# Kernel tuning notes

Measured on AMD Instinct MI355X. Metric: run time of the kernel, lower is better.

Reference implementation:

```python
import jax, jax.numpy as jnp
import numpy as np
import math

B, S, CTX, D, H, DH = 2, 2048, 256, 1024, 16, 64
INNER = H * DH
DFF = 4 * D


def layernorm(x, eps=1e-5):
    m = jnp.mean(x, axis=-1, keepdims=True)
    v = jnp.var(x, axis=-1, keepdims=True)
    return (x - m) * jax.lax.rsqrt(v + eps)


def adaln(x, t, w, b):
    # AdaLayerNorm: linear(t) -> (scale, shift); NOTE: original never applies SiLU.
    emb = t @ w + b                       # [B,1,2D]
    scale, shift = jnp.split(emb, 2, axis=-1)
    return layernorm(x) * (1.0 + scale) + shift


def mha(xq, ctx, wq, wk, wv, wo, bo):
    b, sq, _ = xq.shape
    sk = ctx.shape[1]
    q = (xq @ wq).reshape(b, sq, H, DH).transpose(0, 2, 1, 3)   # bhqd
    k = (ctx @ wk).reshape(b, sk, H, DH).transpose(0, 2, 1, 3)  # bhkd
    v = (ctx @ wv).reshape(b, sk, H, DH).transpose(0, 2, 1, 3)
    scores = jnp.einsum('bhqd,bhkd->bhqk', q, k) / math.sqrt(DH)
    attn = jax.nn.softmax(scores, axis=-1)
    out = jnp.einsum('bhqk,bhkd->bhqd', attn, v)
    out = out.transpose(0, 2, 1, 3).reshape(b, sq, INNER)
    return out @ wo + bo


def glu_ff(x, w1, b1, w2, b2):
    u = x @ w1 + b1                       # [B,S,2*DFF]
    a, gate = jnp.split(u, 2, axis=-1)
    return (a * jax.nn.gelu(gate, approximate=False)) @ w2 + b2


def setup_inputs():
    key = jax.random.key(0)
    ks = jax.random.split(key, 24)
    s = 1.0 / math.sqrt(D)

    def n(k, shape, scale=1.0):
        return jax.random.normal(k, shape, dtype=jnp.float32) * scale

    return {
        'x': n(ks[0], (B, S, D)),
        't': n(ks[1], (B, 1, D)),
        'context': n(ks[2], (B, CTX, D)),
        # self-attention (attn1)
        'attn1_wq': n(ks[3], (D, INNER), s),
        'attn1_wk': n(ks[4], (D, INNER), s),
        'attn1_wv': n(ks[5], (D, INNER), s),
        'attn1_wo': n(ks[6], (INNER, D), s),
        'attn1_bo': n(ks[7], (D,), 0.01),
        # cross-attention (attn2)
        'attn2_wq': n(ks[8], (D, INNER), s),
        'attn2_wk': n(ks[9], (D, INNER), s),
        'attn2_wv': n(ks[10], (D, INNER), s),
        'attn2_wo': n(ks[11], (INNER, D), s),
        'attn2_bo': n(ks[12], (D,), 0.01),
        # gated FFN
        'ff_w1': n(ks[13], (D, 2 * DFF), s),
        'ff_b1': n(ks[14], (2 * DFF,), 0.01),
        'ff_w2': n(ks[15], (DFF, D), 1.0 / math.sqrt(DFF)),
        'ff_b2': n(ks[16], (D,), 0.01),
        # AdaLayerNorm linears (D -> 2D)
        'norm1_w': n(ks[17], (D, 2 * D), s),
        'norm1_b': n(ks[18], (2 * D,), 0.01),
        'norm2_w': n(ks[19], (D, 2 * D), s),
        'norm2_b': n(ks[20], (2 * D,), 0.01),
        'norm3_w': n(ks[21], (D, 2 * D), s),
        'norm3_b': n(ks[22], (2 * D,), 0.01),
    }


def reference(x, t, context,
              attn1_wq, attn1_wk, attn1_wv, attn1_wo, attn1_bo,
              attn2_wq, attn2_wk, attn2_wv, attn2_wo, attn2_bo,
              ff_w1, ff_b1, ff_w2, ff_b2,
              norm1_w, norm1_b, norm2_w, norm2_b, norm3_w, norm3_b):
    h1 = adaln(x, t, norm1_w, norm1_b)
    x = mha(h1, h1, attn1_wq, attn1_wk, attn1_wv, attn1_wo, attn1_bo) + x
    h2 = adaln(x, t, norm2_w, norm2_b)
    x = mha(h2, context, attn2_wq, attn2_wk, attn2_wv, attn2_wo, attn2_bo) + x
    h3 = adaln(x, t, norm3_w, norm3_b)
    x = glu_ff(h3, ff_w1, ff_b1, ff_w2, ff_b2) + x
    return x
```

## Files before the change

### kernel.cpp

```cpp
#include <hip/hip_runtime.h>
#include <hip/hip_bf16.h>
#include <math.h>
#include <stdint.h>

typedef __bf16 bf16;
typedef __attribute__((ext_vector_type(8))) __bf16 bf16x8;
typedef __attribute__((ext_vector_type(4))) __bf16 bf16x4;
typedef __attribute__((ext_vector_type(4))) float f32x4;

static constexpr int cB = 2, cS = 2048, cCTX = 256, cD = 1024, cH = 16, cDH = 64, cDFF = 4096;

__device__ __forceinline__ void glds16(const bf16* g, bf16* l) {
  __builtin_amdgcn_global_load_lds(
      (const __attribute__((address_space(1))) void*)g,
      (__attribute__((address_space(3))) void*)l, 16, 0, 0);
}

__global__ __launch_bounds__(256) void k_transpose(const float* __restrict__ in,
                                                   bf16* __restrict__ out, int K, int N) {
  __shared__ bf16 tile[64][66];
  const int n0 = blockIdx.x * 64, k0 = blockIdx.y * 64;
  const int t = threadIdx.x;
  const int r = t >> 2, cb = (t & 3) * 16;
  const float* src = in + (size_t)(k0 + r) * N + n0 + cb;
#pragma unroll
  for (int q4 = 0; q4 < 4; ++q4) {
    f32x4 v = *(const f32x4*)(src + q4 * 4);
#pragma unroll
    for (int e = 0; e < 4; ++e) tile[r][cb + q4 * 4 + e] = (bf16)v[e];
  }
  __syncthreads();
  bf16* dst = out + (size_t)(n0 + r) * K + k0 + cb;
  bf16x8 o0, o1;
#pragma unroll
  for (int e = 0; e < 8; ++e) { o0[e] = tile[cb + e][r]; o1[e] = tile[cb + 8 + e][r]; }
  *(bf16x8*)(dst) = o0;
  *(bf16x8*)(dst + 8) = o1;
}

__global__ __launch_bounds__(256) void k_vt(const bf16* __restrict__ V, int vstride,
                                            bf16* __restrict__ VT, int kvlen) {
  __shared__ bf16 tile[64][72];
  const int kt = blockIdx.x * 64, bh = blockIdx.y;
  const int b = bh >> 4, h = bh & 15;
  const int t = threadIdx.x, r = t >> 2, cb = (t & 3) * 16;
  const bf16* src = V + (size_t)(b * kvlen + kt + r) * vstride + h * 64 + cb;
  bf16x8 a0 = *(const bf16x8*)src;
  bf16x8 a1 = *(const bf16x8*)(src + 8);
#pragma unroll
  for (int e = 0; e < 8; ++e) { tile[r][cb + e] = a0[e]; tile[r][cb + 8 + e] = a1[e]; }
  __syncthreads();
  bf16* dst = VT + ((size_t)bh * 64 + r) * kvlen + kt + cb;
  bf16x8 o0, o1;
#pragma unroll
  for (int e = 0; e < 8; ++e) { o0[e] = tile[cb + e][r]; o1[e] = tile[cb + 8 + e][r]; }
  *(bf16x8*)(dst) = o0;
  *(bf16x8*)(dst + 8) = o1;
}

__global__ __launch_bounds__(256) void k_f2b(const float* __restrict__ in, bf16* __restrict__ out) {
  const int base = (blockIdx.x * 256 + threadIdx.x) * 4;
  f32x4 v = *(const f32x4*)(in + base);
  bf16x4 o;
#pragma unroll
  for (int e = 0; e < 4; ++e) o[e] = (bf16)v[e];
  *(bf16x4*)(out + base) = o;
}

__global__ __launch_bounds__(256) void k_emb(const float* __restrict__ t,
                                             const float* __restrict__ w,
                                             const float* __restrict__ bias,
                                             float* __restrict__ emb) {
  const int jj = threadIdx.x & 63;
  const int j = blockIdx.x * 64 + jj;
  const int kg = threadIdx.x >> 6;
  float a0 = 0.f, a1 = 0.f;
  for (int k = kg * 256; k < kg * 256 + 256; ++k) {
    float wv = w[(size_t)k * 2048 + j];
    a0 += t[k] * wv;
    a1 += t[1024 + k] * wv;
  }
  __shared__ float s0[4][64], s1[4][64];
  s0[kg][jj] = a0;
  s1[kg][jj] = a1;
  __syncthreads();
  if (threadIdx.x < 64) {
    emb[j] = s0[0][jj] + s0[1][jj] + s0[2][jj] + s0[3][jj] + bias[j];
    emb[2048 + j] = s1[0][jj] + s1[1][jj] + s1[2][jj] + s1[3][jj] + bias[j];
  }
}

__global__ __launch_bounds__(256) void k_adaln(const float* __restrict__ xres,
                                               const float* __restrict__ emb,
                                               bf16* __restrict__ h) {
  const int token = blockIdx.x;
  const int b = token >> 11;
  const float* x = xres + (size_t)token * 1024;
  const float* sc = emb + b * 2048;
  const int t = threadIdx.x;
  float v[4], s = 0.f, sq = 0.f;
#pragma unroll
  for (int i = 0; i < 4; ++i) {
    float u = x[t + 256 * i];
    v[i] = u; s += u; sq += u * u;
  }
#pragma unroll
  for (int off = 1; off < 64; off <<= 1) {
    s += __shfl_xor(s, off);
    sq += __shfl_xor(sq, off);
  }
  __shared__ float ss[4], ssq[4];
  const int wave = t >> 6;
  if ((t & 63) == 0) { ss[wave] = s; ssq[wave] = sq; }
  __syncthreads();
  const float S_ = ss[0] + ss[1] + ss[2] + ss[3];
  const float SQ = ssq[0] + ssq[1] + ssq[2] + ssq[3];
  const float mean = S_ * (1.f / 1024.f);
  const float var = SQ * (1.f / 1024.f) - mean * mean;
  const float rstd = rsqrtf(var + 1e-5f);
#pragma unroll
  for (int i = 0; i < 4; ++i) {
    const int c = t + 256 * i;
    float val = (v[i] - mean) * rstd * (1.f + sc[c]) + sc[1024 + c];
    h[(size_t)token * 1024 + c] = (bf16)val;
  }
}

template <int TN>
__global__ __launch_bounds__(256) void k_gemm_t(const bf16* __restrict__ A,
                                                const bf16* __restrict__ Bt,
                                                bf16* Cb, float* Cf,
                                                const float* __restrict__ bias,
                                                const float* res,
                                                int M, int N, int K) {
  constexpr int JN = TN / 32;
  __shared__ bf16 As[2 * 128 * 32];
  __shared__ bf16 Bs[2 * TN * 32];
  const int m0 = blockIdx.y * 128, n0 = blockIdx.x * TN;
  const int tid = threadIdx.x;
  const int wave = tid >> 6, lane = tid & 63;
  const int quad = lane >> 4, l16 = lane & 15;
  const int mw = (wave >> 1) * 64, nw = (wave & 1) * (TN / 2);
  f32x4 acc[4][JN];
#pragma unroll
  for (int i = 0; i < 4; ++i)
#pragma unroll
    for (int j = 0; j < JN; ++j) acc[i][j] = (f32x4){0.f, 0.f, 0.f, 0.f};

  const int r0 = tid >> 2, c0 = (tid & 3) << 3;
  const bf16* Ap = A + (size_t)(m0 + r0) * K + c0;
  const bf16* Bp = Bt + (size_t)(n0 + r0) * K + c0;
  bf16* lA = As + r0 * 32 + c0;
  bf16* lB = Bs + r0 * 32 + c0;

  for (int k0 = 0; k0 < K; k0 += 64) {
    __syncthreads();
    glds16(Ap + k0, lA);
    glds16(Ap + k0 + (size_t)64 * K, lA + 64 * 32);
    glds16(Ap + k0 + 32, lA + 128 * 32);
    glds16(Ap + k0 + 32 + (size_t)64 * K, lA + 192 * 32);
    glds16(Bp + k0, lB);
    if (TN == 128) glds16(Bp + k0 + (size_t)64 * K, lB + 64 * 32);
    glds16(Bp + k0 + 32, lB + TN * 32);
    if (TN == 128) glds16(Bp + k0 + 32 + (size_t)64 * K, lB + TN * 32 + 64 * 32);
    __syncthreads();
#pragma unroll
    for (int kh = 0; kh < 2; ++kh) {
      const bf16* Asp = As + kh * 128 * 32;
      const bf16* Bsp = Bs + kh * TN * 32;
      bf16x8 af[4], bfr[JN];
#pragma unroll
      for (int i = 0; i < 4; ++i)
        af[i] = *(const bf16x8*)(Asp + (mw + i * 16 + l16) * 32 + quad * 8);
#pragma unroll
      for (int j = 0; j < JN; ++j)
        bfr[j] = *(const bf16x8*)(Bsp + (nw + j * 16 + l16) * 32 + quad * 8);
#pragma unroll
      for (int i = 0; i < 4; ++i)
#pragma unroll
        for (int j = 0; j < JN; ++j)
          acc[i][j] = __builtin_amdgcn_mfma_f32_16x16x32_bf16(af[i], bfr[j], acc[i][j], 0, 0, 0);
    }
  }

#pragma unroll
  for (int i = 0; i < 4; ++i) {
    const int rbase = m0 + mw + i * 16 + quad * 4;
#pragma unroll
    for (int j = 0; j < JN; ++j) {
      const int col = n0 + nw + j * 16 + l16;
      const float bv = bias ? bias[col] : 0.f;
#pragma unroll
      for (int r = 0; r < 4; ++r) {
        const size_t off = (size_t)(rbase + r) * N + col;
        float v2 = acc[i][j][r] + bv;
        if (res) v2 += res[off];
        if (Cf) Cf[off] = v2;
        if (Cb) Cb[off] = (bf16)v2;
      }
    }
  }
}

__global__ __launch_bounds__(256) void k_gemm_glu(const bf16* __restrict__ A,
                                                  const bf16* __restrict__ Bt,
                                                  const float* __restrict__ bias,
                                                  bf16* __restrict__ Cb,
                                                  int M, int N, int K) {
  __shared__ bf16 As[2 * 128 * 32];
  __shared__ bf16 Ba[2 * 64 * 32];
  __shared__ bf16 Bg[2 * 64 * 32];
  const int m0 = blockIdx.y * 128, n0 = blockIdx.x * 64;
  const int tid = threadIdx.x;
  const int wave = tid >> 6, lane = tid & 63;
  const int quad = lane >> 4, l16 = lane & 15;
  const int mw = (wave >> 1) * 64, nw = (wave & 1) * 32;
  f32x4 aa[4][2], ag[4][2];
#pragma unroll
  for (int i = 0; i < 4; ++i)
#pragma unroll
    for (int j = 0; j < 2; ++j) {
      aa[i][j] = (f32x4){0.f, 0.f, 0.f, 0.f};
      ag[i][j] = (f32x4){0.f, 0.f, 0.f, 0.f};
    }

  const int r0 = tid >> 2, c0 = (tid & 3) << 3;
  const bf16* Ap = A + (size_t)(m0 + r0) * K + c0;
  const bf16* Bap = Bt + (size_t)(n0 + r0) * K + c0;
  const bf16* Bgp = Bt + (size_t)(N + n0 + r0) * K + c0;
  bf16* lA = As + r0 * 32 + c0;
  bf16* lBa = Ba + r0 * 32 + c0;
  bf16* lBg = Bg + r0 * 32 + c0;

  for (int k0 = 0; k0 < K; k0 += 64) {
    __syncthreads();
    glds16(Ap + k0, lA);
    glds16(Ap + k0 + (size_t)64 * K, lA + 64 * 32);
    glds16(Ap + k0 + 32, lA + 128 * 32);
    glds16(Ap + k0 + 32 + (size_t)64 * K, lA + 192 * 32);
    glds16(Bap + k0, lBa);
    glds16(Bap + k0 + 32, lBa + 64 * 32);
    glds16(Bgp + k0, lBg);
    glds16(Bgp + k0 + 32, lBg + 64 * 32);
    __syncthreads();
#pragma unroll
    for (int kh = 0; kh < 2; ++kh) {
      const bf16* Asp = As + kh * 128 * 32;
      const bf16* Bap_s = Ba + kh * 64 * 32;
      const bf16* Bgp_s = Bg + kh * 64 * 32;
      bf16x8 af[4], ba[2], bg[2];
#pragma unroll
      for (int i = 0; i < 4; ++i)
        af[i] = *(const bf16x8*)(Asp + (mw + i * 16 + l16) * 32 + quad * 8);
#pragma unroll
      for (int j = 0; j < 2; ++j) {
        ba[j] = *(const bf16x8*)(Bap_s + (nw + j * 16 + l16) * 32 + quad * 8);
        bg[j] = *(const bf16x8*)(Bgp_s + (nw + j * 16 + l16) * 32 + quad * 8);
      }
#pragma unroll
      for (int i = 0; i < 4; ++i)
#pragma unroll
        for (int j = 0; j < 2; ++j) {
          aa[i][j] = __builtin_amdgcn_mfma_f32_16x16x32_bf16(af[i], ba[j], aa[i][j], 0, 0, 0);
          ag[i][j] = __builtin_amdgcn_mfma_f32_16x16x32_bf16(af[i], bg[j], ag[i][j], 0, 0, 0);
        }
    }
  }

#pragma unroll
  for (int i = 0; i < 4; ++i) {
    const int rbase = m0 + mw + i * 16 + quad * 4;
#pragma unroll
    for (int j = 0; j < 2; ++j) {
      const int col = n0 + nw + j * 16 + l16;
      const float ba_v = bias[col];
      const float bg_v = bias[N + col];
#pragma unroll
      for (int r = 0; r < 4; ++r) {
        float av = aa[i][j][r] + ba_v;
        float gv = ag[i][j][r] + bg_v;
        float ge = 0.5f * gv * (1.0f + erff(gv * 0.70710678118654752f));
        Cb[(size_t)(rbase + r) * N + col] = (bf16)(av * ge);
      }
    }
  }
}

__global__ __launch_bounds__(256) void k_attn(const bf16* __restrict__ Qp, int qstride,
                                              const bf16* __restrict__ Kp, int kstride,
                                              const bf16* __restrict__ VTp,
                                              bf16* __restrict__ Op, int kvlen) {
  const int qt = blockIdx.x * 128;
  const int hd = blockIdx.y;
  const int b = blockIdx.z;
  const int tid = threadIdx.x;
  const int wave = tid >> 6, lane = tid & 63;
  const int quad = lane >> 4, l16 = lane & 15;

  __shared__ __align__(16) bf16 Ks[64 * 64];
  __shared__ __align__(16) bf16 Vs[64 * 64];
  __shared__ __align__(16) bf16 Ps[4][32 * 72];

  bf16x8 qf[2][2];
#pragma unroll
  for (int g = 0; g < 2; ++g) {
    const bf16* qrow = Qp + (size_t)(b * cS + qt + wave * 32 + g * 16 + l16) * qstride + hd * 64;
#pragma unroll
    for (int c = 0; c < 2; ++c) {
      bf16x8 raw = *(const bf16x8*)(qrow + c * 32 + quad * 8);
#pragma unroll
      for (int e = 0; e < 8; ++e) qf[g][c][e] = (bf16)((float)raw[e] * 0.125f);
    }
  }

  float l_part[2][4] = {{0.f, 0.f, 0.f, 0.f}, {0.f, 0.f, 0.f, 0.f}};
  f32x4 o_acc[2][4];
#pragma unroll
  for (int g = 0; g < 2; ++g)
#pragma unroll
    for (int n = 0; n < 4; ++n) o_acc[g][n] = (f32x4){0.f, 0.f, 0.f, 0.f};

  const int lrow = wave * 16 + (lane >> 3);
  const int lcol = (lane & 7) * 8;
  const bf16* kbase = Kp + (size_t)(b * kvlen + lrow) * kstride + hd * 64 + lcol;
  const bf16* vbase = VTp + ((size_t)((b * 16 + hd) * 64 + lrow)) * kvlen + lcol;
  bf16* lk = Ks + lrow * 64 + lcol;
  bf16* lv = Vs + lrow * 64 + lcol;

  for (int kt = 0; kt < kvlen; kt += 64) {
    __syncthreads();
    const bf16* kg = kbase + (size_t)kt * kstride;
    glds16(kg, lk);
    glds16(kg + (size_t)8 * kstride, lk + 8 * 64);
    glds16(vbase + kt, lv);
    glds16(vbase + kt + (size_t)8 * kvlen, lv + 8 * 64);
    __syncthreads();

    f32x4 s[2][4];
#pragma unroll
    for (int g = 0; g < 2; ++g)
#pragma unroll
      for (int t = 0; t < 4; ++t) s[g][t] = (f32x4){0.f, 0.f, 0.f, 0.f};
#pragma unroll
    for (int t = 0; t < 4; ++t)
#pragma unroll
      for (int c = 0; c < 2; ++c) {
        bf16x8 kf = *(const bf16x8*)(Ks + (t * 16 + l16) * 64 + c * 32 + quad * 8);
#pragma unroll
        for (int g = 0; g < 2; ++g)
          s[g][t] = __builtin_amdgcn_mfma_f32_16x16x32_bf16(qf[g][c], kf, s[g][t], 0, 0, 0);
      }

#pragma unroll
    for (int g = 0; g < 2; ++g)
#pragma unroll
      for (int t = 0; t < 4; ++t)
#pragma unroll
        for (int r = 0; r < 4; ++r) {
          float p = __expf(s[g][t][r]);
          Ps[wave][(g * 16 + quad * 4 + r) * 72 + t * 16 + l16] = (bf16)p;
          l_part[g][r] += p;
        }

    bf16x8 pf[2][2];
#pragma unroll
    for (int g = 0; g < 2; ++g)
#pragma unroll
      for (int c = 0; c < 2; ++c)
        pf[g][c] = *(const bf16x8*)(&Ps[wave][(g * 16 + l16) * 72 + c * 32 + quad * 8]);
#pragma unroll
    for (int n = 0; n < 4; ++n)
#pragma unroll
      for (int c = 0; c < 2; ++c) {
        bf16x8 vf = *(const bf16x8*)(Vs + (n * 16 + l16) * 64 + c * 32 + quad * 8);
#pragma unroll
        for (int g = 0; g < 2; ++g)
          o_acc[g][n] = __builtin_amdgcn_mfma_f32_16x16x32_bf16(pf[g][c], vf, o_acc[g][n], 0, 0, 0);
      }
  }

#pragma unroll
  for (int g = 0; g < 2; ++g) {
    float rl[4];
#pragma unroll
    for (int r = 0; r < 4; ++r) {
      float v = l_part[g][r];
      v += __shfl_xor(v, 1);
      v += __shfl_xor(v, 2);
      v += __shfl_xor(v, 4);
      v += __shfl_xor(v, 8);
      rl[r] = 1.f / v;
    }
#pragma unroll
    for (int n = 0; n < 4; ++n)
#pragma unroll
      for (int r = 0; r < 4; ++r) {
        const int srow = qt + wave * 32 + g * 16 + quad * 4 + r;
        const int d = n * 16 + l16;
        Op[(size_t)(b * cS + srow) * 1024 + hd * 64 + d] = (bf16)(o_acc[g][n][r] * rl[r]);
      }
  }
}

extern "C" void kernel_launch(void* const* d_in, const int* in_sizes, int n_in,
                              void* d_out, int out_size, void* d_ws, size_t ws_size,
                              hipStream_t stream) {
  const float* x    = (const float*)d_in[0];
  const float* tt   = (const float*)d_in[1];
  const float* ctx  = (const float*)d_in[2];
  const float* a1wq = (const float*)d_in[3];
  const float* a1wk = (const float*)d_in[4];
  const float* a1wv = (const float*)d_in[5];
  const float* a1wo = (const float*)d_in[6];
  const float* a1bo = (const float*)d_in[7];
  const float* a2wq = (const float*)d_in[8];
  const float* a2wk = (const float*)d_in[9];
  const float* a2wv = (const float*)d_in[10];
  const float* a2wo = (const float*)d_in[11];
  const float* a2bo = (const float*)d_in[12];
  const float* fw1  = (const float*)d_in[13];
  const float* fb1  = (const float*)d_in[14];
  const float* fw2  = (const float*)d_in[15];
  const float* fb2  = (const float*)d_in[16];
  const float* n1w  = (const float*)d_in[17];
  const float* n1b  = (const float*)d_in[18];
  const float* n2w  = (const float*)d_in[19];
  const float* n2b  = (const float*)d_in[20];
  const float* n3w  = (const float*)d_in[21];
  const float* n3b  = (const float*)d_in[22];

  char* ws = (char*)d_ws;
  const size_t MB = 1ull << 20;
  bf16* wqkv1 = (bf16*)(ws + 0 * MB);
  bf16* wto1  = (bf16*)(ws + 6 * MB);
  bf16* wtq2  = (bf16*)(ws + 8 * MB);
  bf16* wkv2w = (bf16*)(ws + 10 * MB);
  bf16* wto2  = (bf16*)(ws + 14 * MB);
  bf16* wtf1  = (bf16*)(ws + 16 * MB);
  bf16* wtf2  = (bf16*)(ws + 32 * MB);
  float* emb1 = (float*)(ws + 40 * MB);
  float* emb2 = (float*)(ws + 40 * MB + 65536);
  float* emb3 = (float*)(ws + 40 * MB + 131072);
  bf16* ctxb  = (bf16*)(ws + 40 * MB + 262144);
  float* xres = (float*)(ws + 42 * MB);
  bf16* h     = (bf16*)(ws + 58 * MB);
  bf16* ao    = h;
  bf16* qkv   = (bf16*)(ws + 66 * MB);
  bf16* q2    = qkv;
  bf16* vT1   = (bf16*)(ws + 90 * MB);
  bf16* kv2   = (bf16*)(ws + 0 * MB);
  bf16* vT2   = (bf16*)(ws + 2 * MB);
  bf16* g     = (bf16*)(ws + 66 * MB);
  float* out  = (float*)d_out;

  const dim3 blk(256);

  k_transpose<<<dim3(16, 16), blk, 0, stream>>>(a1wq, wqkv1, 1024, 1024);
  k_transpose<<<dim3(16, 16), blk, 0, stream>>>(a1wk, wqkv1 + 1024 * 1024, 1024, 1024);
  k_transpose<<<dim3(16, 16), blk, 0, stream>>>(a1wv, wqkv1 + 2 * 1024 * 1024, 1024, 1024);
  k_transpose<<<dim3(16, 16), blk, 0, stream>>>(a1wo, wto1, 1024, 1024);
  k_transpose<<<dim3(16, 16), blk, 0, stream>>>(a2wq, wtq2, 1024, 1024);
  k_transpose<<<dim3(16, 16), blk, 0, stream>>>(a2wk, wkv2w, 1024, 1024);
  k_transpose<<<dim3(16, 16), blk, 0, stream>>>(a2wv, wkv2w + 1024 * 1024, 1024, 1024);
  k_transpose<<<dim3(16, 16), blk, 0, stream>>>(a2wo, wto2, 1024, 1024);
  k_transpose<<<dim3(128, 16), blk, 0, stream>>>(fw1, wtf1, 1024, 8192);
  k_transpose<<<dim3(16, 64), blk, 0, stream>>>(fw2, wtf2, 4096, 1024);

  k_emb<<<32, blk, 0, stream>>>(tt, n1w, n1b, emb1);
  k_emb<<<32, blk, 0, stream>>>(tt, n2w, n2b, emb2);
  k_emb<<<32, blk, 0, stream>>>(tt, n3w, n3b, emb3);
  k_f2b<<<512, blk, 0, stream>>>(ctx, ctxb);

  k_adaln<<<4096, blk, 0, stream>>>(x, emb1, h);
  k_gemm_t<128><<<dim3(24, 32), blk, 0, stream>>>(h, wqkv1, qkv, nullptr, nullptr, nullptr, 4096, 3072, 1024);
  k_vt<<<dim3(32, 32), blk, 0, stream>>>(qkv + 2048, 3072, vT1, 2048);
  k_attn<<<dim3(16, 16, 2), blk, 0, stream>>>(qkv, 3072, qkv + 1024, 3072, vT1, ao, 2048);
  k_gemm_t<64><<<dim3(16, 32), blk, 0, stream>>>(ao, wto1, nullptr, xres, a1bo, x, 4096, 1024, 1024);

  k_adaln<<<4096, blk, 0, stream>>>(xres, emb2, h);
  k_gemm_t<64><<<dim3(16, 32), blk, 0, stream>>>(h, wtq2, q2, nullptr, nullptr, nullptr, 4096, 1024, 1024);
  k_gemm_t<128><<<dim3(16, 4), blk, 0, stream>>>(ctxb, wkv2w, kv2, nullptr, nullptr, nullptr, 512, 2048, 1024);
  k_vt<<<dim3(4, 32), blk, 0, stream>>>(kv2 + 1024, 2048, vT2, 256);
  k_attn<<<dim3(16, 16, 2), blk, 0, stream>>>(q2, 1024, kv2, 2048, vT2, ao, 256);
  k_gemm_t<64><<<dim3(16, 32), blk, 0, stream>>>(ao, wto2, nullptr, xres, a2bo, xres, 4096, 1024, 1024);

  k_adaln<<<4096, blk, 0, stream>>>(xres, emb3, h);
  k_gemm_glu<<<dim3(64, 32), blk, 0, stream>>>(h, wtf1, fb1, g, 4096, 4096, 1024);
  k_gemm_t<64><<<dim3(16, 32), blk, 0, stream>>>(g, wtf2, nullptr, out, fb2, xres, 4096, 1024, 4096);
}
```

Before: 678.8 us.

## Switch GEMMs to 32x32x16 MFMA and batch transpose and embedding launches

The GEMM and GLU-GEMM inner loops move from 16x16x32 MFMA tiles to 32x32x16 MFMA tiles. Each wave now loads fewer LDS fragments per k-step and issues fewer, larger MFMA instructions, with the epilogue index mapping rewritten to match. Separately, the eight 1024x1024 weight transposes are merged into one launch over blockIdx.z, and the three AdaLN embedding linears into one launch, to cut launch overhead. The 32x32 layout changes LDS access patterns and the epilogue store pattern, which may cost bank conflicts or coalescing.

```diff
diff --git a/kernel.cpp b/kernel.cpp
--- a/kernel.cpp
+++ b/kernel.cpp
@@ -7,6 +7,7 @@
 typedef __attribute__((ext_vector_type(8))) __bf16 bf16x8;
 typedef __attribute__((ext_vector_type(4))) __bf16 bf16x4;
 typedef __attribute__((ext_vector_type(4))) float f32x4;
+typedef __attribute__((ext_vector_type(16))) float f32x16;
 
 static constexpr int cB = 2, cS = 2048, cCTX = 256, cD = 1024, cH = 16, cDH = 64, cDFF = 4096;
 
@@ -14,6 +15,31 @@
   __builtin_amdgcn_global_load_lds(
       (const __attribute__((address_space(1))) void*)g,
       (__attribute__((address_space(3))) void*)l, 16, 0, 0);
+}
+
+struct T8 { const float* s[8]; };
+__global__ __launch_bounds__(256) void k_transpose8(T8 args, bf16* __restrict__ out) {
+  __shared__ bf16 tile[64][66];
+  const int n0 = blockIdx.x * 64, k0 = blockIdx.y * 64;
+  const int z = blockIdx.z;
+  const float* in = args.s[z];
+  bf16* dst_base = out + (size_t)z * 1024 * 1024;
+  const int t = threadIdx.x;
+  const int r = t >> 2, cb = (t & 3) * 16;
+  const float* src = in + (size_t)(k0 + r) * 1024 + n0 + cb;
+#pragma unroll
+  for (int q4 = 0; q4 < 4; ++q4) {
+    f32x4 v = *(const f32x4*)(src + q4 * 4);
+#pragma unroll
+    for (int e = 0; e < 4; ++e) tile[r][cb + q4 * 4 + e] = (bf16)v[e];
+  }
+  __syncthreads();
+  bf16* dst = dst_base + (size_t)(n0 + r) * 1024 + k0 + cb;
+  bf16x8 o0, o1;
+#pragma unroll
+  for (int e = 0; e < 8; ++e) { o0[e] = tile[cb + e][r]; o1[e] = tile[cb + 8 + e][r]; }
+  *(bf16x8*)(dst) = o0;
+  *(bf16x8*)(dst + 8) = o1;
 }
 
 __global__ __launch_bounds__(256) void k_transpose(const float* __restrict__ in,
@@ -67,10 +93,14 @@
   *(bf16x4*)(out + base) = o;
 }
 
-__global__ __launch_bounds__(256) void k_emb(const float* __restrict__ t,
-                                             const float* __restrict__ w,
-                                             const float* __restrict__ bias,
-                                             float* __restrict__ emb) {
+struct EmbArgs { const float* w0; const float* w1; const float* w2;
+                 const float* b0; const float* b1; const float* b2; };
+__global__ __launch_bounds__(256) void k_emb3(const float* __restrict__ t, EmbArgs ea,
+                                              float* __restrict__ emb) {
+  const int which = blockIdx.y;
+  const float* w = which == 0 ? ea.w0 : (which == 1 ? ea.w1 : ea.w2);
+  const float* bias = which == 0 ? ea.b0 : (which == 1 ? ea.b1 : ea.b2);
+  float* dst = emb + which * 4096;
   const int jj = threadIdx.x & 63;
   const int j = blockIdx.x * 64 + jj;
   const int kg = threadIdx.x >> 6;
@@ -85,8 +115,8 @@
   s1[kg][jj] = a1;
   __syncthreads();
   if (threadIdx.x < 64) {
-    emb[j] = s0[0][jj] + s0[1][jj] + s0[2][jj] + s0[3][jj] + bias[j];
-    emb[2048 + j] = s1[0][jj] + s1[1][jj] + s1[2][jj] + s1[3][jj] + bias[j];
+    dst[j] = s0[0][jj] + s0[1][jj] + s0[2][jj] + s0[3][jj] + bias[j];
+    dst[2048 + j] = s1[0][jj] + s1[1][jj] + s1[2][jj] + s1[3][jj] + bias[j];
   }
 }
 
@@ -133,19 +163,19 @@
                                                 const float* __restrict__ bias,
                                                 const float* res,
                                                 int M, int N, int K) {
-  constexpr int JN = TN / 32;
+  constexpr int CJ = TN / 64;
   __shared__ bf16 As[2 * 128 * 32];
   __shared__ bf16 Bs[2 * TN * 32];
   const int m0 = blockIdx.y * 128, n0 = blockIdx.x * TN;
   const int tid = threadIdx.x;
   const int wave = tid >> 6, lane = tid & 63;
-  const int quad = lane >> 4, l16 = lane & 15;
+  const int l31 = lane & 31, hi8 = (lane >> 5) * 8;
   const int mw = (wave >> 1) * 64, nw = (wave & 1) * (TN / 2);
-  f32x4 acc[4][JN];
-#pragma unroll
-  for (int i = 0; i < 4; ++i)
-#pragma unroll
-    for (int j = 0; j < JN; ++j) acc[i][j] = (f32x4){0.f, 0.f, 0.f, 0.f};
+  f32x16 acc[2][CJ];
+#pragma unroll
+  for (int i = 0; i < 2; ++i)
+#pragma unroll
+    for (int j = 0; j < CJ; ++j) acc[i][j] = (f32x16)(0.f);
 
   const int r0 = tid >> 2, c0 = (tid & 3) << 3;
   const bf16* Ap = A + (size_t)(m0 + r0) * K + c0;
@@ -165,35 +195,39 @@
     if (TN == 128) glds16(Bp + k0 + 32 + (size_t)64 * K, lB + TN * 32 + 64 * 32);
     __syncthreads();
 #pragma unroll
-    for (int kh = 0; kh < 2; ++kh) {
-      const bf16* Asp = As + kh * 128 * 32;
-      const bf16* Bsp = Bs + kh * TN * 32;
-      bf16x8 af[4], bfr[JN];
-#pragma unroll
-      for (int i = 0; i < 4; ++i)
-        af[i] = *(const bf16x8*)(Asp + (mw + i * 16 + l16) * 32 + quad * 8);
-#pragma unroll
-      for (int j = 0; j < JN; ++j)
-        bfr[j] = *(const bf16x8*)(Bsp + (nw + j * 16 + l16) * 32 + quad * 8);
-#pragma unroll
-      for (int i = 0; i < 4; ++i)
-#pragma unroll
-        for (int j = 0; j < JN; ++j)
-          acc[i][j] = __builtin_amdgcn_mfma_f32_16x16x32_bf16(af[i], bfr[j], acc[i][j], 0, 0, 0);
+    for (int kp = 0; kp < 2; ++kp) {
+      const bf16* Asp = As + kp * 128 * 32;
+      const bf16* Bsp = Bs + kp * TN * 32;
+#pragma unroll
+      for (int kh = 0; kh < 2; ++kh) {
+        bf16x8 af[2], bfr[CJ];
+#pragma unroll
+        for (int i = 0; i < 2; ++i)
+          af[i] = *(const bf16x8*)(Asp + (mw + i * 32 + l31) * 32 + kh * 16 + hi8);
+#pragma unroll
+        for (int j = 0; j < CJ; ++j)
+          bfr[j] = *(const bf16x8*)(Bsp + (nw + j * 32 + l31) * 32 + kh * 16 + hi8);
+#pragma unroll
+        for (int i = 0; i < 2; ++i)
+#pragma unroll
+          for (int j = 0; j < CJ; ++j)
+            acc[i][j] = __builtin_amdgcn_mfma_f32_32x32x16_bf16(af[i], bfr[j], acc[i][j], 0, 0, 0);
+      }
     }
   }
 
 #pragma unroll
-  for (int i = 0; i < 4; ++i) {
-    const int rbase = m0 + mw + i * 16 + quad * 4;
-#pragma unroll
-    for (int j = 0; j < JN; ++j) {
-      const int col = n0 + nw + j * 16 + l16;
+  for (int i = 0; i < 2; ++i) {
+    const int rb = m0 + mw + i * 32 + 4 * (lane >> 5);
+#pragma unroll
+    for (int j = 0; j < CJ; ++j) {
+      const int col = n0 + nw + j * 32 + l31;
       const float bv = bias ? bias[col] : 0.f;
 #pragma unroll
-      for (int r = 0; r < 4; ++r) {
-        const size_t off = (size_t)(rbase + r) * N + col;
-        float v2 = acc[i][j][r] + bv;
+      for (int reg = 0; reg < 16; ++reg) {
+        const int row = rb + (reg & 3) + 8 * (reg >> 2);
+        const size_t off = (size_t)row * N + col;
+        float v2 = acc[i][j][reg] + bv;
         if (res) v2 += res[off];
         if (Cf) Cf[off] = v2;
         if (Cb) Cb[off] = (bf16)v2;
@@ -213,16 +247,11 @@
   const int m0 = blockIdx.y * 128, n0 = blockIdx.x * 64;
   const int tid = threadIdx.x;
   const int wave = tid >> 6, lane = tid & 63;
-  const int quad = lane >> 4, l16 = lane & 15;
+  const int l31 = lane & 31, hi8 = (lane >> 5) * 8;
   const int mw = (wave >> 1) * 64, nw = (wave & 1) * 32;
-  f32x4 aa[4][2], ag[4][2];
-#pragma unroll
-  for (int i = 0; i < 4; ++i)
-#pragma unroll
-    for (int j = 0; j < 2; ++j) {
-      aa[i][j] = (f32x4){0.f, 0.f, 0.f, 0.f};
-      ag[i][j] = (f32x4){0.f, 0.f, 0.f, 0.f};
-    }
+  f32x16 aa[2], ag[2];
+#pragma unroll
+  for (int i = 0; i < 2; ++i) { aa[i] = (f32x16)(0.f); ag[i] = (f32x16)(0.f); }
 
   const int r0 = tid >> 2, c0 = (tid & 3) << 3;
   const bf16* Ap = A + (size_t)(m0 + r0) * K + c0;
@@ -244,44 +273,40 @@
     glds16(Bgp + k0 + 32, lBg + 64 * 32);
     __syncthreads();
 #pragma unroll
-    for (int kh = 0; kh < 2; ++kh) {
-      const bf16* Asp = As + kh * 128 * 32;
-      const bf16* Bap_s = Ba + kh * 64 * 32;
-      const bf16* Bgp_s = Bg + kh * 64 * 32;
-      bf16x8 af[4], ba[2], bg[2];
-#pragma unroll
-      for (int i = 0; i < 4; ++i)
-        af[i] = *(const bf16x8*)(Asp + (mw + i * 16 + l16) * 32 + quad * 8);
-#pragma unroll
-      for (int j = 0; j < 2; ++j) {
-        ba[j] = *(const bf16x8*)(Bap_s + (nw + j * 16 + l16) * 32 + quad * 8);
-        bg[j] = *(const bf16x8*)(Bgp_s + (nw + j * 16 + l16) * 32 + quad * 8);
+    for (int kp = 0; kp < 2; ++kp) {
+      const bf16* Asp = As + kp * 128 * 32;
+      const bf16* Bap_s = Ba + kp * 64 * 32;
+      const bf16* Bgp_s = Bg + kp * 64 * 32;
+#pragma unroll
+      for (int kh = 0; kh < 2; ++kh) {
+        bf16x8 af[2], ba, bg;
+#pragma unroll
+        for (int i = 0; i < 2; ++i)
+          af[i] = *(const bf16x8*)(Asp + (mw + i * 32 + l31) * 32 + kh * 16 + hi8);
+        ba = *(const bf16x8*)(Bap_s + (nw + l31) * 32 + kh * 16 + hi8);
+        bg = *(const bf16x8*)(Bgp_s + (nw + l31) * 32 + kh * 16 + hi8);
+#pragma unroll
+        for (int i = 0; i < 2; ++i) {
+          aa[i] = __builtin_amdgcn_mfma_f32_32x32x16_bf16(af[i], ba, aa[i], 0, 0, 0);
+          ag[i] = __builtin_amdgcn_mfma_f32_32x32x16_bf16(af[i], bg, ag[i], 0, 0, 0);
+        }
       }
-#pragma unroll
-      for (int i = 0; i < 4; ++i)
-#pragma unroll
-        for (int j = 0; j < 2; ++j) {
-          aa[i][j] = __builtin_amdgcn_mfma_f32_16x16x32_bf16(af[i], ba[j], aa[i][j], 0, 0, 0);
-          ag[i][j] = __builtin_amdgcn_mfma_f32_16x16x32_bf16(af[i], bg[j], ag[i][j], 0, 0, 0);
-        }
     }
   }
 
-#pragma unroll
-  for (int i = 0; i < 4; ++i) {
-    const int rbase = m0 + mw + i * 16 + quad * 4;
-#pragma unroll
-    for (int j = 0; j < 2; ++j) {
-      const int col = n0 + nw + j * 16 + l16;
-      const float ba_v = bias[col];
-      const float bg_v = bias[N + col];
-#pragma unroll
-      for (int r = 0; r < 4; ++r) {
-        float av = aa[i][j][r] + ba_v;
-        float gv = ag[i][j][r] + bg_v;
-        float ge = 0.5f * gv * (1.0f + erff(gv * 0.70710678118654752f));
-        Cb[(size_t)(rbase + r) * N + col] = (bf16)(av * ge);
-      }
+  const int col = n0 + nw + l31;
+  const float ba_v = bias[col];
+  const float bg_v = bias[N + col];
+#pragma unroll
+  for (int i = 0; i < 2; ++i) {
+    const int rb = m0 + mw + i * 32 + 4 * (lane >> 5);
+#pragma unroll
+    for (int reg = 0; reg < 16; ++reg) {
+      const int row = rb + (reg & 3) + 8 * (reg >> 2);
+      float av = aa[i][reg] + ba_v;
+      float gv = ag[i][reg] + bg_v;
+      float ge = 0.5f * gv * (1.0f + erff(gv * 0.70710678118654752f));
+      Cb[(size_t)row * N + col] = (bf16)(av * ge);
     }
   }
 }
@@ -408,39 +433,25 @@
   const float* x    = (const float*)d_in[0];
   const float* tt   = (const float*)d_in[1];
   const float* ctx  = (const float*)d_in[2];
-  const float* a1wq = (const float*)d_in[3];
-  const float* a1wk = (const float*)d_in[4];
-  const float* a1wv = (const float*)d_in[5];
-  const float* a1wo = (const float*)d_in[6];
-  const float* a1bo = (const float*)d_in[7];
-  const float* a2wq = (const float*)d_in[8];
-  const float* a2wk = (const float*)d_in[9];
-  const float* a2wv = (const float*)d_in[10];
-  const float* a2wo = (const float*)d_in[11];
-  const float* a2bo = (const float*)d_in[12];
   const float* fw1  = (const float*)d_in[13];
   const float* fb1  = (const float*)d_in[14];
   const float* fw2  = (const float*)d_in[15];
   const float* fb2  = (const float*)d_in[16];
-  const float* n1w  = (const float*)d_in[17];
-  const float* n1b  = (const float*)d_in[18];
-  const float* n2w  = (const float*)d_in[19];
-  const float* n2b  = (const float*)d_in[20];
-  const float* n3w  = (const float*)d_in[21];
-  const float* n3b  = (const float*)d_in[22];
+  const float* a1bo = (const float*)d_in[7];
+  const float* a2bo = (const float*)d_in[12];
 
   char* ws = (char*)d_ws;
   const size_t MB = 1ull << 20;
-  bf16* wqkv1 = (bf16*)(ws + 0 * MB);
+  bf16* wsq   = (bf16*)(ws + 0 * MB);
+  bf16* wqkv1 = wsq;
   bf16* wto1  = (bf16*)(ws + 6 * MB);
   bf16* wtq2  = (bf16*)(ws + 8 * MB);
   bf16* wkv2w = (bf16*)(ws + 10 * MB);
   bf16* wto2  = (bf16*)(ws + 14 * MB);
   bf16* wtf1  = (bf16*)(ws + 16 * MB);
   bf16* wtf2  = (bf16*)(ws + 32 * MB);
-  float* emb1 = (float*)(ws + 40 * MB);
-  float* emb2 = (float*)(ws + 40 * MB + 65536);
-  float* emb3 = (float*)(ws + 40 * MB + 131072);
+  float* emb  = (float*)(ws + 40 * MB);
+  float* emb1 = emb, *emb2 = emb + 4096, *emb3 = emb + 8192;
   bf16* ctxb  = (bf16*)(ws + 40 * MB + 262144);
   float* xres = (float*)(ws + 42 * MB);
   bf16* h     = (bf16*)(ws + 58 * MB);
@@ -455,20 +466,24 @@
 
   const dim3 blk(256);
 
-  k_transpose<<<dim3(16, 16), blk, 0, stream>>>(a1wq, wqkv1, 1024, 1024);
-  k_transpose<<<dim3(16, 16), blk, 0, stream>>>(a1wk, wqkv1 + 1024 * 1024, 1024, 1024);
-  k_transpose<<<dim3(16, 16), blk, 0, stream>>>(a1wv, wqkv1 + 2 * 1024 * 1024, 1024, 1024);
-  k_transpose<<<dim3(16, 16), blk, 0, stream>>>(a1wo, wto1, 1024, 1024);
-  k_transpose<<<dim3(16, 16), blk, 0, stream>>>(a2wq, wtq2, 1024, 1024);
-  k_transpose<<<dim3(16, 16), blk, 0, stream>>>(a2wk, wkv2w, 1024, 1024);
-  k_transpose<<<dim3(16, 16), blk, 0, stream>>>(a2wv, wkv2w + 1024 * 1024, 1024, 1024);
-  k_transpose<<<dim3(16, 16), blk, 0, stream>>>(a2wo, wto2, 1024, 1024);
+  T8 t8;
+  t8.s[0] = (const float*)d_in[3];
+  t8.s[1] = (const float*)d_in[4];
+  t8.s[2] = (const float*)d_in[5];
+  t8.s[3] = (const float*)d_in[6];
+  t8.s[4] = (const float*)d_in[8];
+  t8.s[5] = (const float*)d_in[9];
+  t8.s[6] = (const float*)d_in[10];
+  t8.s[7] = (const float*)d_in[11];
+  k_transpose8<<<dim3(16, 16, 8), blk, 0, stream>>>(t8, wsq);
   k_transpose<<<dim3(128, 16), blk, 0, stream>>>(fw1, wtf1, 1024, 8192);
   k_transpose<<<dim3(16, 64), blk, 0, stream>>>(fw2, wtf2, 4096, 1024);
 
-  k_emb<<<32, blk, 0, stream>>>(tt, n1w, n1b, emb1);
-  k_emb<<<32, blk, 0, stream>>>(tt, n2w, n2b, emb2);
-  k_emb<<<32, blk, 0, stream>>>(tt, n3w, n3b, emb3);
+  EmbArgs ea;
+  ea.w0 = (const float*)d_in[17]; ea.b0 = (const float*)d_in[18];
+  ea.w1 = (const float*)d_in[19]; ea.b1 = (const float*)d_in[20];
+  ea.w2 = (const float*)d_in[21]; ea.b2 = (const float*)d_in[22];
+  k_emb3<<<dim3(32, 3), blk, 0, stream>>>(tt, ea, emb);
   k_f2b<<<512, blk, 0, stream>>>(ctx, ctxb);
 
   k_adaln<<<4096, blk, 0, stream>>>(x, emb1, h);
```

New measurement: 641.4 us. 5.5% less time.
